# Kernel tuning notes

Measured on AMD Instinct MI355X. Metric: run time of the kernel, lower is better.

Reference implementation:

```python
import jax, jax.numpy as jnp
import numpy as np

DIM = 512

def setup_inputs() -> dict:
    key = jax.random.key(0)
    ks = jax.random.split(key, 10)
    B, N, D = 8, 4096, DIM
    s = 1.0 / np.sqrt(D)
    return {
        "x": jax.random.normal(ks[0], (B, N, D), dtype=jnp.float32),
        "wq": jax.random.normal(ks[1], (D, D), dtype=jnp.float32) * s,
        "bq": jnp.zeros((D,), dtype=jnp.float32),
        "wk": jax.random.normal(ks[2], (D, D), dtype=jnp.float32) * s,
        "bk": jnp.zeros((D,), dtype=jnp.float32),
        "wp": jax.random.normal(ks[3], (D, D), dtype=jnp.float32) * s,
        "bp": jnp.zeros((D,), dtype=jnp.float32),
        "wf": jax.random.normal(ks[4], (D, D), dtype=jnp.float32) * s,
        "bf": jnp.zeros((D,), dtype=jnp.float32),
        "w_g": jax.random.normal(ks[5], (D, 1), dtype=jnp.float32),
    }

def reference(x, wq, bq, wk, bk, wp, bp, wf, bf, w_g):
    D = x.shape[-1]
    scale = D ** (-0.5)
    query = x @ wq + bq                      # [B,N,D]
    key_t = x @ wk + bk                      # [B,N,D]
    # l2 normalize along last dim (tf.math.l2_normalize uses eps=1e-12 via rsqrt of max(sum_sq, eps))
    def l2n(t):
        ss = jnp.sum(t * t, axis=-1, keepdims=True)
        return t * jax.lax.rsqrt(jnp.maximum(ss, 1e-12))
    query = l2n(query)
    key_t = l2n(key_t)
    query_weight = query @ w_g               # [B,N,1]
    scaled = query_weight * scale
    # Faithful to TF code: softmax over axis=-1 of a size-1 axis -> all ones
    attn = jax.nn.softmax(scaled, axis=-1)   # [B,N,1] == 1.0
    global_queries = jnp.sum(attn * query, axis=1)  # [B,D]
    gq = global_queries[:, None, :]          # broadcast over N (tile)
    out = (gq * key_t) @ wp + bp + query     # [B,N,D]
    out = out @ wf + bf
    return out
```

## Files before the change

### kernel.cpp

```cpp
#include <hip/hip_runtime.h>
#include <stdint.h>

typedef __bf16 bf16x8 __attribute__((ext_vector_type(8)));
typedef float floatx4 __attribute__((ext_vector_type(4)));
typedef unsigned short u16;
typedef u16 u16x8 __attribute__((ext_vector_type(8)));

__device__ __forceinline__ float bf2f(u16 u) {
    union { uint32_t i; float f; } v; v.i = ((uint32_t)u) << 16; return v.f;
}
__device__ __forceinline__ u16 f2bf(float f) {
    union { float f; uint32_t i; } v; v.f = f;
    uint32_t r = v.i + 0x7fffu + ((v.i >> 16) & 1u);
    return (u16)(r >> 16);
}

__device__ __forceinline__ void gload_lds16(const u16* g, u16* l) {
    __builtin_amdgcn_global_load_lds(
        (const __attribute__((address_space(1))) void*)g,
        (__attribute__((address_space(3))) void*)l,
        16, 0, 0);
}

#define BK 64

__global__ __launch_bounds__(512, 2) void gemm1_kernel(
    const u16* __restrict__ A,
    const u16* __restrict__ Bt,
    const float* __restrict__ bias,
    float* __restrict__ ssq_out,
    u16* __restrict__ C16)
{
    __shared__ __attribute__((aligned(16))) u16 lds[2 * 32768];
    const int tid  = threadIdx.x;
    const int wave = tid >> 6;
    const int lane = tid & 63;
    const int quad = lane >> 4;
    const int l16  = lane & 15;
    const int wm = wave >> 2, wn = wave & 3;

    const int gx   = gridDim.x;
    const int nwg  = gx * gridDim.y;
    const int wgid = blockIdx.y * gx + blockIdx.x;
    const int cpx  = nwg >> 3;
    const int swz  = (wgid & 7) * cpx + (wgid >> 3);
    const int row0 = (swz / gx) * 256;
    const int col0 = (swz % gx) * 256;

    floatx4 acc[8][4] = {};

    const int rsub = lane >> 3;
    const int ksub = ((lane & 7) ^ rsub) << 3;
    const u16* aptr[4]; const u16* bptr[4];
#pragma unroll
    for (int c = 0; c < 4; ++c) {
        const int cc = wave * 4 + c;
        aptr[c] = A  + (size_t)(row0 + cc * 8 + rsub) * 512 + ksub;
        bptr[c] = Bt + (size_t)(col0 + cc * 8 + rsub) * 512 + ksub;
    }
    const int NT = 8;

#define STAGE1(T, B)                                                          \
    {                                                                         \
        u16* dA_ = &lds[(B) * 32768];                                         \
        u16* dB_ = dA_ + 16384;                                               \
        const int kt_ = (T) * BK;                                             \
        _Pragma("unroll")                                                     \
        for (int c = 0; c < 4; ++c) {                                         \
            const int cc = wave * 4 + c;                                      \
            gload_lds16(aptr[c] + kt_, dA_ + cc * 512);                       \
            gload_lds16(bptr[c] + kt_, dB_ + cc * 512);                       \
        }                                                                     \
    }

    STAGE1(0, 0);
    STAGE1(1, 1);
    for (int t = 0; t < NT; ++t) {
        if (t + 1 < NT) asm volatile("s_waitcnt vmcnt(8)" ::: "memory");
        else            asm volatile("s_waitcnt vmcnt(0)" ::: "memory");
        __builtin_amdgcn_s_barrier();
        __builtin_amdgcn_sched_barrier(0);
        const u16* sA = &lds[(t & 1) * 32768];
        const u16* sB = sA + 16384;
#pragma unroll
        for (int ks = 0; ks < 2; ++ks) {
            const int pgo = (((ks * 4 + quad) ^ (l16 & 7)) << 3);
            bf16x8 bfr[4];
#pragma unroll
            for (int n = 0; n < 4; ++n)
                bfr[n] = *(const bf16x8*)&sB[(wn * 64 + n * 16 + l16) * 64 + pgo];
            __builtin_amdgcn_s_setprio(1);
#pragma unroll
            for (int m = 0; m < 8; ++m) {
                bf16x8 af = *(const bf16x8*)&sA[(wm * 128 + m * 16 + l16) * 64 + pgo];
#pragma unroll
                for (int n = 0; n < 4; ++n)
                    acc[m][n] = __builtin_amdgcn_mfma_f32_16x16x32_bf16(af, bfr[n], acc[m][n], 0, 0, 0);
            }
            __builtin_amdgcn_s_setprio(0);
        }
        __builtin_amdgcn_sched_barrier(0);
        asm volatile("" ::: "memory");
        __builtin_amdgcn_s_barrier();
        asm volatile("" ::: "memory");
        if (t + 2 < NT) STAGE1(t + 2, t & 1);
    }
#undef STAGE1

    u16* til = lds;
#pragma unroll
    for (int h = 0; h < 2; ++h) {
        __syncthreads();
        if (wm == h) {
            float bv[4];
#pragma unroll
            for (int n = 0; n < 4; ++n) bv[n] = bias[col0 + wn * 64 + n * 16 + l16];
#pragma unroll
            for (int m = 0; m < 8; ++m) {
                int rowl = m * 16 + quad * 4;
#pragma unroll
                for (int n = 0; n < 4; ++n) {
                    int tcol = wn * 64 + n * 16 + l16;
#pragma unroll
                    for (int t = 0; t < 4; ++t)
                        til[(rowl + t) * 264 + tcol] = f2bf(acc[m][n][t] + bv[n]);
                }
            }
        }
        __syncthreads();
        float ssl[8];
#pragma unroll
        for (int c = 0; c < 8; ++c) {
            int r  = c * 16 + (tid >> 5);
            int cu = (tid & 31) * 8;
            ushort4 lo = *(const ushort4*)&til[r * 264 + cu];
            ushort4 hi = *(const ushort4*)&til[r * 264 + cu + 4];
            u16x8 o;
            o[0] = lo.x; o[1] = lo.y; o[2] = lo.z; o[3] = lo.w;
            o[4] = hi.x; o[5] = hi.y; o[6] = hi.z; o[7] = hi.w;
            *(u16x8*)&C16[(size_t)(row0 + h * 128 + r) * 1024 + col0 + cu] = o;
            float ss = 0.f;
#pragma unroll
            for (int q2 = 0; q2 < 8; ++q2) { float f = bf2f(o[q2]); ss += f * f; }
            ssl[c] = ss;
        }
        float* so = ssq_out + (size_t)(col0 >> 9) * 32768 + row0 + h * 128;
#pragma unroll
        for (int c = 0; c < 8; ++c) {
            float s = ssl[c];
            s += __shfl_xor(s, 1);
            s += __shfl_xor(s, 2);
            s += __shfl_xor(s, 4);
            s += __shfl_xor(s, 8);
            s += __shfl_xor(s, 16);
            if ((lane & 31) == 0) atomicAdd(&so[c * 16 + (tid >> 5)], s);
        }
    }
}

__global__ __launch_bounds__(512, 2) void gemm_qk_kernel(
    const u16* __restrict__ A,
    const u16* __restrict__ BtF,
    const u16* __restrict__ BtPF,
    const float* __restrict__ bpf,
    const float* __restrict__ ssqQ,
    const float* __restrict__ ssqK,
    float* __restrict__ C32)
{
    __shared__ __attribute__((aligned(16))) u16 lds[2 * 32768];
    const int tid  = threadIdx.x;
    const int wave = tid >> 6;
    const int lane = tid & 63;
    const int quad = lane >> 4;
    const int l16  = lane & 15;
    const int wm = wave >> 2, wn = wave & 3;

    const int gx   = gridDim.x;
    const int nwg  = gx * gridDim.y;
    const int wgid = blockIdx.y * gx + blockIdx.x;
    const int cpx  = nwg >> 3;
    const int swz  = (wgid & 7) * cpx + (wgid >> 3);
    const int row0 = (swz / gx) * 256;
    const int col0 = (swz % gx) * 256;
    const int batch = row0 >> 12;

    floatx4 acc[8][4] = {};

    const int rsub = lane >> 3;
    const int ksub = ((lane & 7) ^ rsub) << 3;
    const u16* aptr[4]; const u16* bptrF[4]; const u16* bptrP[4];
    const u16* BP = BtPF + (size_t)batch * 262144;
#pragma unroll
    for (int c = 0; c < 4; ++c) {
        const int cc = wave * 4 + c;
        aptr[c]  = A   + (size_t)(row0 + cc * 8 + rsub) * 1024 + ksub;
        bptrF[c] = BtF + (size_t)(col0 + cc * 8 + rsub) * 512  + ksub;
        bptrP[c] = BP  + (size_t)(col0 + cc * 8 + rsub) * 512  + ksub;
    }
    const int NT = 16;

#define STAGEQ(T, B)                                                          \
    {                                                                         \
        u16* dA_ = &lds[(B) * 32768];                                         \
        u16* dB_ = dA_ + 16384;                                               \
        const int kt_ = (T) * BK;                                             \
        _Pragma("unroll")                                                     \
        for (int c = 0; c < 4; ++c) {                                         \
            const int cc = wave * 4 + c;                                      \
            gload_lds16(aptr[c] + kt_, dA_ + cc * 512);                       \
            const u16* bsrc_ = (kt_ < 512) ? (bptrF[c] + kt_)                 \
                                           : (bptrP[c] + (kt_ - 512));        \
            gload_lds16(bsrc_, dB_ + cc * 512);                               \
        }                                                                     \
    }

    STAGEQ(0, 0);
    STAGEQ(1, 1);
    for (int t = 0; t < NT; ++t) {
        if (t + 1 < NT) asm volatile("s_waitcnt vmcnt(8)" ::: "memory");
        else            asm volatile("s_waitcnt vmcnt(0)" ::: "memory");
        __builtin_amdgcn_s_barrier();
        __builtin_amdgcn_sched_barrier(0);
        const u16* sA = &lds[(t & 1) * 32768];
        const u16* sB = sA + 16384;
#pragma unroll
        for (int ks = 0; ks < 2; ++ks) {
            const int pgo = (((ks * 4 + quad) ^ (l16 & 7)) << 3);
            bf16x8 bfr[4];
#pragma unroll
            for (int n = 0; n < 4; ++n)
                bfr[n] = *(const bf16x8*)&sB[(wn * 64 + n * 16 + l16) * 64 + pgo];
            __builtin_amdgcn_s_setprio(1);
#pragma unroll
            for (int m = 0; m < 8; ++m) {
                bf16x8 af = *(const bf16x8*)&sA[(wm * 128 + m * 16 + l16) * 64 + pgo];
#pragma unroll
                for (int n = 0; n < 4; ++n)
                    acc[m][n] = __builtin_amdgcn_mfma_f32_16x16x32_bf16(af, bfr[n], acc[m][n], 0, 0, 0);
            }
            __builtin_amdgcn_s_setprio(0);
        }
        if (t == 7) {
#pragma unroll
            for (int m = 0; m < 8; ++m) {
                int rowb = row0 + wm * 128 + m * 16 + quad * 4;
                float4 q4 = *(const float4*)&ssqQ[rowb];
                float4 k4 = *(const float4*)&ssqK[rowb];
                float ratio[4];
                ratio[0] = rsqrtf(fmaxf(q4.x, 1e-12f)) / rsqrtf(fmaxf(k4.x, 1e-12f));
                ratio[1] = rsqrtf(fmaxf(q4.y, 1e-12f)) / rsqrtf(fmaxf(k4.y, 1e-12f));
                ratio[2] = rsqrtf(fmaxf(q4.z, 1e-12f)) / rsqrtf(fmaxf(k4.z, 1e-12f));
                ratio[3] = rsqrtf(fmaxf(q4.w, 1e-12f)) / rsqrtf(fmaxf(k4.w, 1e-12f));
#pragma unroll
                for (int n = 0; n < 4; ++n)
#pragma unroll
                    for (int tt = 0; tt < 4; ++tt)
                        acc[m][n][tt] *= ratio[tt];
            }
        }
        __builtin_amdgcn_sched_barrier(0);
        asm volatile("" ::: "memory");
        __builtin_amdgcn_s_barrier();
        asm volatile("" ::: "memory");
        if (t + 2 < NT) STAGEQ(t + 2, t & 1);
    }
#undef STAGEQ

    float* ftile = (float*)lds;
#pragma unroll
    for (int p = 0; p < 4; ++p) {
        __syncthreads();
        if (wm == (p >> 1)) {
            float bv[4];
#pragma unroll
            for (int n = 0; n < 4; ++n) bv[n] = bpf[col0 + wn * 64 + n * 16 + l16];
#pragma unroll
            for (int mi = 0; mi < 4; ++mi) {
                int m = (p & 1) * 4 + mi;
                int rowl = mi * 16 + quad * 4;
                int rowb = row0 + p * 64 + rowl;
                float4 k4 = *(const float4*)&ssqK[rowb];
                float rsk4[4];
                rsk4[0] = rsqrtf(fmaxf(k4.x, 1e-12f));
                rsk4[1] = rsqrtf(fmaxf(k4.y, 1e-12f));
                rsk4[2] = rsqrtf(fmaxf(k4.z, 1e-12f));
                rsk4[3] = rsqrtf(fmaxf(k4.w, 1e-12f));
#pragma unroll
                for (int n = 0; n < 4; ++n) {
                    int tcol = wn * 64 + n * 16 + l16;
#pragma unroll
                    for (int t = 0; t < 4; ++t)
                        ftile[(rowl + t) * 264 + tcol] = acc[m][n][t] * rsk4[t] + bv[n];
                }
            }
        }
        __syncthreads();
#pragma unroll
        for (int c = 0; c < 8; ++c) {
            int r  = c * 8 + wave;
            int cu = lane * 4;
            float4 v = *(const float4*)&ftile[r * 264 + cu];
            *(float4*)&C32[(size_t)(row0 + p * 64 + r) * 512 + col0 + cu] = v;
        }
    }
}

__global__ __launch_bounds__(256) void gsum_p_kernel(
    const u16* __restrict__ QK, const float* __restrict__ ssqQ, float* __restrict__ g,
    const u16* __restrict__ BtF, const u16* __restrict__ wpb, u16* __restrict__ Pt)
{
    __shared__ __attribute__((aligned(16))) char shmem[128 * 132 * 2];
    const int tid  = threadIdx.x;
    const int lane = tid & 63;
    const int wave = tid >> 6;

    if (blockIdx.x < 256) {
        float (*gtile)[512] = (float(*)[512])shmem;
        const int row0 = blockIdx.x * 128 + wave * 32;
        const int batch = row0 >> 12;
        const int d = lane * 8;
        float gacc[8] = {};
        for (int rr = 0; rr < 32; ++rr) {
            int row = row0 + rr;
            float s = rsqrtf(fmaxf(ssqQ[row], 1e-12f));
            u16x8 q = *(const u16x8*)(QK + (size_t)row * 1024 + d);
#pragma unroll
            for (int i = 0; i < 8; ++i) gacc[i] += s * bf2f(q[i]);
        }
#pragma unroll
        for (int i = 0; i < 8; ++i) gtile[wave][d + i] = gacc[i];
        __syncthreads();
        int c2 = tid * 2;
        float s0 = gtile[0][c2]     + gtile[1][c2]     + gtile[2][c2]     + gtile[3][c2];
        float s1 = gtile[0][c2 + 1] + gtile[1][c2 + 1] + gtile[2][c2 + 1] + gtile[3][c2 + 1];
        atomicAdd(&g[batch * 512 + c2], s0);
        atomicAdd(&g[batch * 512 + c2 + 1], s1);
        return;
    }

    u16* lds  = (u16*)shmem;
    u16* lsA  = lds;
    u16* lsB  = lds + 128 * BK;
    const int quad = lane >> 4;
    const int l16  = lane & 15;
    const int wm = wave >> 1, wn = wave & 1;
    const int bid2 = blockIdx.x - 256;
    const int row0 = (bid2 >> 2) * 128;
    const int col0 = (bid2 & 3) * 128;

    floatx4 acc[4][4] = {};
    const int rsub = lane >> 3;
    const int ksub = ((lane & 7) ^ rsub) << 3;
    const u16* aptr[4]; const u16* bptr[4];
#pragma unroll
    for (int c = 0; c < 4; ++c) {
        const int cc = wave * 4 + c;
        aptr[c] = BtF + (size_t)(row0 + cc * 8 + rsub) * 512 + ksub;
        bptr[c] = wpb + (size_t)(col0 + cc * 8 + rsub) * 512 + ksub;
    }
    for (int kt = 0; kt < 512; kt += BK) {
#pragma unroll
        for (int c = 0; c < 4; ++c) {
            const int cc = wave * 4 + c;
            gload_lds16(aptr[c] + kt, &lsA[cc * 512]);
            gload_lds16(bptr[c] + kt, &lsB[cc * 512]);
        }
        __syncthreads();
#pragma unroll
        for (int ks = 0; ks < 2; ++ks) {
            const int pgo = (((ks * 4 + quad) ^ (l16 & 7)) << 3);
            bf16x8 af[4], bfr[4];
#pragma unroll
            for (int i = 0; i < 4; ++i)
                af[i] = *(const bf16x8*)&lsA[(wm * 64 + i * 16 + l16) * BK + pgo];
#pragma unroll
            for (int j = 0; j < 4; ++j)
                bfr[j] = *(const bf16x8*)&lsB[(wn * 64 + j * 16 + l16) * BK + pgo];
#pragma unroll
            for (int i = 0; i < 4; ++i)
#pragma unroll
                for (int j = 0; j < 4; ++j)
                    acc[i][j] = __builtin_amdgcn_mfma_f32_16x16x32_bf16(af[i], bfr[j], acc[i][j], 0, 0, 0);
        }
        __syncthreads();
    }
#pragma unroll
    for (int j = 0; j < 4; ++j) {
        int tcol = wn * 64 + j * 16 + l16;
#pragma unroll
        for (int i = 0; i < 4; ++i) {
            int trow = wm * 64 + i * 16 + quad * 4;
#pragma unroll
            for (int t = 0; t < 4; ++t)
                lds[(trow + t) * 132 + tcol] = f2bf(acc[i][j][t]);
        }
    }
    __syncthreads();
#pragma unroll
    for (int c = 0; c < 8; ++c) {
        int r  = c * 16 + (tid >> 4);
        int cu = (tid & 15) * 8;
        ushort4 lo = *(const ushort4*)&lds[r * 132 + cu];
        ushort4 hi = *(const ushort4*)&lds[r * 132 + cu + 4];
        u16x8 o;
        o[0] = lo.x; o[1] = lo.y; o[2] = lo.z; o[3] = lo.w;
        o[4] = hi.x; o[5] = hi.y; o[6] = hi.z; o[7] = hi.w;
        *(u16x8*)&Pt[(size_t)(row0 + r) * 512 + col0 + cu] = o;
    }
}

__global__ __launch_bounds__(256) void scalePF_kernel(const u16* __restrict__ Pt,
                                                      const float* __restrict__ g,
                                                      u16* __restrict__ BtPF)
{
    size_t i8 = ((size_t)blockIdx.x * 256 + threadIdx.x) * 8;
    int b   = (int)(i8 >> 18);
    int rem = (int)(i8 & 262143);
    int kk  = rem & 511;
    u16x8 p = *(const u16x8*)(Pt + rem);
    float4 g0 = *(const float4*)(g + b * 512 + kk);
    float4 g1 = *(const float4*)(g + b * 512 + kk + 4);
    u16x8 o;
    o[0] = f2bf(bf2f(p[0]) * g0.x); o[1] = f2bf(bf2f(p[1]) * g0.y);
    o[2] = f2bf(bf2f(p[2]) * g0.z); o[3] = f2bf(bf2f(p[3]) * g0.w);
    o[4] = f2bf(bf2f(p[4]) * g1.x); o[5] = f2bf(bf2f(p[5]) * g1.y);
    o[6] = f2bf(bf2f(p[6]) * g1.z); o[7] = f2bf(bf2f(p[7]) * g1.w);
    *(u16x8*)(BtPF + (size_t)b * 262144 + rem) = o;
}

__global__ __launch_bounds__(256) void prep_kernel(
    const float* __restrict__ x,  u16* __restrict__ xb,
    const float* __restrict__ wq, const float* __restrict__ wk, const float* __restrict__ wf,
    u16* __restrict__ Bt1, u16* __restrict__ BtF,
    const float* __restrict__ wp, u16* __restrict__ wpb,
    const float* __restrict__ bq, const float* __restrict__ bk, float* __restrict__ biasQK,
    const float* __restrict__ bp, const float* __restrict__ bfv, float* __restrict__ bpf)
{
    __shared__ u16 tile[32][34];
    const int bid = blockIdx.x;
    const int tid = threadIdx.x;

    if (bid < 16384) {
        size_t i = ((size_t)bid * 256 + tid) * 4;
        float4 v = *(const float4*)(x + i);
        ushort4 o;
        o.x = f2bf(v.x); o.y = f2bf(v.y); o.z = f2bf(v.z); o.w = f2bf(v.w);
        *(ushort4*)(xb + i) = o;
    } else if (bid < 17152) {
        const int tb = bid - 16384;
        const int which = tb >> 8;
        const float* W = (which == 0) ? wq : (which == 1) ? wk : wf;
        u16* Bt = (which == 0) ? Bt1 : (which == 1) ? (Bt1 + 512 * 512) : BtF;
        const int b2 = tb & 255;
        const int tk = b2 & 15;
        const int tn = b2 >> 4;
        const int c  = tid & 31;
        const int r0 = tid >> 5;
#pragma unroll
        for (int i = 0; i < 4; ++i) {
            int r = r0 + i * 8;
            tile[r][c] = f2bf(W[(size_t)(tk * 32 + r) * 512 + tn * 32 + c]);
        }
        __syncthreads();
#pragma unroll
        for (int i = 0; i < 4; ++i) {
            int r = r0 + i * 8;
            Bt[(size_t)(tn * 32 + r) * 512 + tk * 32 + c] = tile[c][r];
        }
    } else if (bid < 17408) {
        size_t i = ((size_t)(bid - 17152) * 256 + tid) * 4;
        float4 v = *(const float4*)(wp + i);
        ushort4 o;
        o.x = f2bf(v.x); o.y = f2bf(v.y); o.z = f2bf(v.z); o.w = f2bf(v.w);
        *(ushort4*)(wpb + i) = o;
    } else if (bid < 17412) {
        int id = (bid - 17408) * 256 + tid;
        biasQK[id] = (id < 512) ? bq[id] : bk[id - 512];
    } else {
        const int bb = bid - 17412;
        const int j0 = bb * 32;
        float s0 = 0.f, s1 = 0.f;
#pragma unroll 4
        for (int j = j0; j < j0 + 32; ++j) {
            s0 += bp[j] * wf[(size_t)j * 512 + tid];
            s1 += bp[j] * wf[(size_t)j * 512 + tid + 256];
        }
        if (bb == 0) { s0 += bfv[tid]; s1 += bfv[tid + 256]; }
        atomicAdd(&bpf[tid], s0);
        atomicAdd(&bpf[tid + 256], s1);
    }
}

extern "C" void kernel_launch(void* const* d_in, const int* in_sizes, int n_in,
                              void* d_out, int out_size, void* d_ws, size_t ws_size,
                              hipStream_t stream)
{
    const float* x  = (const float*)d_in[0];
    const float* wq = (const float*)d_in[1];
    const float* bq = (const float*)d_in[2];
    const float* wk = (const float*)d_in[3];
    const float* bk = (const float*)d_in[4];
    const float* wp = (const float*)d_in[5];
    const float* bp = (const float*)d_in[6];
    const float* wf = (const float*)d_in[7];
    const float* bf = (const float*)d_in[8];

    char* ws = (char*)d_ws;
    u16*   xb     = (u16*)(ws);
    u16*   QK     = (u16*)(ws + 33554432);
    u16*   Bt1    = (u16*)(ws + 100663296);
    u16*   BtF    = (u16*)(ws + 101711872);
    u16*   wpb    = (u16*)(ws + 102236160);
    u16*   Pt     = (u16*)(ws + 102760448);
    u16*   BtPF   = (u16*)(ws + 103284736);
    float* biasQK = (float*)(ws + 107479040);
    float* g      = (float*)(ws + 107483136);
    float* ssq    = (float*)(ws + 107499520);
    float* bpf    = (float*)(ws + 107761664);

    hipMemsetAsync(g, 0, 280576, stream);
    prep_kernel<<<17428, 256, 0, stream>>>(x, xb, wq, wk, wf, Bt1, BtF, wp, wpb,
                                           bq, bk, biasQK, bp, bf, bpf);
    gemm1_kernel<<<dim3(4, 128), 512, 0, stream>>>(xb, Bt1, biasQK, ssq, QK);
    gsum_p_kernel<<<272, 256, 0, stream>>>(QK, ssq, g, BtF, wpb, Pt);
    scalePF_kernel<<<1024, 256, 0, stream>>>(Pt, g, BtPF);
    gemm_qk_kernel<<<dim3(2, 128), 512, 0, stream>>>(QK, BtF, BtPF, bpf, ssq, ssq + 32768, (float*)d_out);
}
```

Measured before the change: 244.3 us.

## Fuse fp32-to-bf16 conversion of x into the first GEMM's A-tile load

Removes the separate pass that converted x to bf16 in the prep kernel. The first GEMM now reads fp32 x directly through registers, converts it to bf16 and writes it to LDS, while B still uses direct global-to-LDS loads. This saves writing and re-reading a 32 MB bf16 copy of x. In exchange the GEMM's pipeline becomes register-staged with __syncthreads, and occupancy drops to 1 block per CU because of the extra registers, so load/compute overlap may be weaker.

New measurement: 246.3 us. No clear change (+0.8%).

```diff
diff --git a/kernel.cpp b/kernel.cpp
--- a/kernel.cpp
+++ b/kernel.cpp
@@ -24,8 +24,8 @@
 
 #define BK 64
 
-__global__ __launch_bounds__(512, 2) void gemm1_kernel(
-    const u16* __restrict__ A,
+__global__ __launch_bounds__(512, 1) void gemm1_kernel(
+    const float* __restrict__ X,
     const u16* __restrict__ Bt,
     const float* __restrict__ bias,
     float* __restrict__ ssq_out,
@@ -50,36 +50,50 @@
     floatx4 acc[8][4] = {};
 
     const int rsub = lane >> 3;
-    const int ksub = ((lane & 7) ^ rsub) << 3;
-    const u16* aptr[4]; const u16* bptr[4];
+    const int s8   = ((lane & 7) ^ rsub) << 3;
+    const float* aptr[4]; const u16* bptr[4];
 #pragma unroll
     for (int c = 0; c < 4; ++c) {
         const int cc = wave * 4 + c;
-        aptr[c] = A  + (size_t)(row0 + cc * 8 + rsub) * 512 + ksub;
-        bptr[c] = Bt + (size_t)(col0 + cc * 8 + rsub) * 512 + ksub;
+        aptr[c] = X  + (size_t)(row0 + cc * 8 + rsub) * 512 + s8;
+        bptr[c] = Bt + (size_t)(col0 + cc * 8 + rsub) * 512 + s8;
     }
     const int NT = 8;
-
-#define STAGE1(T, B)                                                          \
-    {                                                                         \
-        u16* dA_ = &lds[(B) * 32768];                                         \
-        u16* dB_ = dA_ + 16384;                                               \
-        const int kt_ = (T) * BK;                                             \
-        _Pragma("unroll")                                                     \
-        for (int c = 0; c < 4; ++c) {                                         \
-            const int cc = wave * 4 + c;                                      \
-            gload_lds16(aptr[c] + kt_, dA_ + cc * 512);                       \
-            gload_lds16(bptr[c] + kt_, dB_ + cc * 512);                       \
-        }                                                                     \
-    }
-
-    STAGE1(0, 0);
-    STAGE1(1, 1);
+    float4 av[4][2];
+
+#define LOADA(T)                                                              \
+    _Pragma("unroll")                                                         \
+    for (int c = 0; c < 4; ++c) {                                             \
+        av[c][0] = *(const float4*)(aptr[c] + (T) * BK);                      \
+        av[c][1] = *(const float4*)(aptr[c] + (T) * BK + 4);                  \
+    }
+#define LOADB(T, B)                                                           \
+    _Pragma("unroll")                                                         \
+    for (int c = 0; c < 4; ++c)                                               \
+        gload_lds16(bptr[c] + (T) * BK, &lds[(B) * 32768 + 16384 + (wave * 4 + c) * 512]);
+#define WRITEA(B)                                                             \
+    _Pragma("unroll")                                                         \
+    for (int c = 0; c < 4; ++c) {                                             \
+        bf16x8 o;                                                             \
+        union { u16 u; __bf16 b; } cv;                                        \
+        cv.u = f2bf(av[c][0].x); o[0] = cv.b;                                 \
+        cv.u = f2bf(av[c][0].y); o[1] = cv.b;                                 \
+        cv.u = f2bf(av[c][0].z); o[2] = cv.b;                                 \
+        cv.u = f2bf(av[c][0].w); o[3] = cv.b;                                 \
+        cv.u = f2bf(av[c][1].x); o[4] = cv.b;                                 \
+        cv.u = f2bf(av[c][1].y); o[5] = cv.b;                                 \
+        cv.u = f2bf(av[c][1].z); o[6] = cv.b;                                 \
+        cv.u = f2bf(av[c][1].w); o[7] = cv.b;                                 \
+        *(bf16x8*)&lds[(B) * 32768 + (wave * 4 + c) * 512 + lane * 8] = o;    \
+    }
+
+    LOADA(0);
+    LOADB(0, 0);
+    WRITEA(0);
+    __syncthreads();
+
     for (int t = 0; t < NT; ++t) {
-        if (t + 1 < NT) asm volatile("s_waitcnt vmcnt(8)" ::: "memory");
-        else            asm volatile("s_waitcnt vmcnt(0)" ::: "memory");
-        __builtin_amdgcn_s_barrier();
-        __builtin_amdgcn_sched_barrier(0);
+        if (t + 1 < NT) { LOADA(t + 1); LOADB(t + 1, (t + 1) & 1); }
         const u16* sA = &lds[(t & 1) * 32768];
         const u16* sB = sA + 16384;
 #pragma unroll
@@ -99,13 +113,12 @@
             }
             __builtin_amdgcn_s_setprio(0);
         }
-        __builtin_amdgcn_sched_barrier(0);
-        asm volatile("" ::: "memory");
-        __builtin_amdgcn_s_barrier();
-        asm volatile("" ::: "memory");
-        if (t + 2 < NT) STAGE1(t + 2, t & 1);
-    }
-#undef STAGE1
+        if (t + 1 < NT) WRITEA((t + 1) & 1);
+        __syncthreads();
+    }
+#undef LOADA
+#undef LOADB
+#undef WRITEA
 
     u16* til = lds;
 #pragma unroll
@@ -428,8 +441,7 @@
     *(u16x8*)(BtPF + (size_t)b * 262144 + rem) = o;
 }
 
-__global__ __launch_bounds__(256) void prep_kernel(
-    const float* __restrict__ x,  u16* __restrict__ xb,
+__global__ __launch_bounds__(256) void prep_w_kernel(
     const float* __restrict__ wq, const float* __restrict__ wk, const float* __restrict__ wf,
     u16* __restrict__ Bt1, u16* __restrict__ BtF,
     const float* __restrict__ wp, u16* __restrict__ wpb,
@@ -440,18 +452,11 @@
     const int bid = blockIdx.x;
     const int tid = threadIdx.x;
 
-    if (bid < 16384) {
-        size_t i = ((size_t)bid * 256 + tid) * 4;
-        float4 v = *(const float4*)(x + i);
-        ushort4 o;
-        o.x = f2bf(v.x); o.y = f2bf(v.y); o.z = f2bf(v.z); o.w = f2bf(v.w);
-        *(ushort4*)(xb + i) = o;
-    } else if (bid < 17152) {
-        const int tb = bid - 16384;
-        const int which = tb >> 8;
+    if (bid < 768) {
+        const int which = bid >> 8;
         const float* W = (which == 0) ? wq : (which == 1) ? wk : wf;
         u16* Bt = (which == 0) ? Bt1 : (which == 1) ? (Bt1 + 512 * 512) : BtF;
-        const int b2 = tb & 255;
+        const int b2 = bid & 255;
         const int tk = b2 & 15;
         const int tn = b2 >> 4;
         const int c  = tid & 31;
@@ -467,17 +472,17 @@
             int r = r0 + i * 8;
             Bt[(size_t)(tn * 32 + r) * 512 + tk * 32 + c] = tile[c][r];
         }
-    } else if (bid < 17408) {
-        size_t i = ((size_t)(bid - 17152) * 256 + tid) * 4;
+    } else if (bid < 1024) {
+        size_t i = ((size_t)(bid - 768) * 256 + tid) * 4;
         float4 v = *(const float4*)(wp + i);
         ushort4 o;
         o.x = f2bf(v.x); o.y = f2bf(v.y); o.z = f2bf(v.z); o.w = f2bf(v.w);
         *(ushort4*)(wpb + i) = o;
-    } else if (bid < 17412) {
-        int id = (bid - 17408) * 256 + tid;
+    } else if (bid < 1028) {
+        int id = (bid - 1024) * 256 + tid;
         biasQK[id] = (id < 512) ? bq[id] : bk[id - 512];
     } else {
-        const int bb = bid - 17412;
+        const int bb = bid - 1028;
         const int j0 = bb * 32;
         float s0 = 0.f, s1 = 0.f;
 #pragma unroll 4
@@ -506,7 +511,6 @@
     const float* bf = (const float*)d_in[8];
 
     char* ws = (char*)d_ws;
-    u16*   xb     = (u16*)(ws);
     u16*   QK     = (u16*)(ws + 33554432);
     u16*   Bt1    = (u16*)(ws + 100663296);
     u16*   BtF    = (u16*)(ws + 101711872);
@@ -519,9 +523,9 @@
     float* bpf    = (float*)(ws + 107761664);
 
     hipMemsetAsync(g, 0, 280576, stream);
-    prep_kernel<<<17428, 256, 0, stream>>>(x, xb, wq, wk, wf, Bt1, BtF, wp, wpb,
-                                           bq, bk, biasQK, bp, bf, bpf);
-    gemm1_kernel<<<dim3(4, 128), 512, 0, stream>>>(xb, Bt1, biasQK, ssq, QK);
+    prep_w_kernel<<<1044, 256, 0, stream>>>(wq, wk, wf, Bt1, BtF, wp, wpb,
+                                            bq, bk, biasQK, bp, bf, bpf);
+    gemm1_kernel<<<dim3(4, 128), 512, 0, stream>>>(x, Bt1, biasQK, ssq, QK);
     gsum_p_kernel<<<272, 256, 0, stream>>>(QK, ssq, g, BtF, wpb, Pt);
     scalePF_kernel<<<1024, 256, 0, stream>>>(Pt, g, BtPF);
     gemm_qk_kernel<<<dim3(2, 128), 512, 0, stream>>>(QK, BtF, BtPF, bpf, ssq, ssq + 32768, (float*)d_out);
```
